# Kernel optimization log

Hardware: AMD Instinct MI355X
Metric: run time of the kernel (lower is better)

The kernel has to match this reference:

```python
import jax, jax.numpy as jnp
import numpy as np

N = 128      # n_ab: number of independent tiny MLPs
H = 128      # hidden width
L = 4097     # odd alpha grid length, alpha[L//2] == pi/2


def setup_inputs() -> dict:
    key = jax.random.key(0)
    ks = jax.random.split(key, 10)
    alpha = jnp.linspace(0.0, np.pi, L).astype(jnp.float32)
    s = 1.0 / np.sqrt(H)
    w0 = jax.random.normal(ks[0], (N, H, 1), dtype=jnp.float32) * 0.5
    w1 = jax.random.normal(ks[1], (N, H, H), dtype=jnp.float32) * s
    w2 = jax.random.normal(ks[2], (N, H, H), dtype=jnp.float32) * s
    w3 = jax.random.normal(ks[3], (N, 1, H), dtype=jnp.float32) * s
    b0 = jax.random.normal(ks[4], (N, H), dtype=jnp.float32) * 0.1
    b1 = jax.random.normal(ks[5], (N, H), dtype=jnp.float32) * 0.1
    b2 = jax.random.normal(ks[6], (N, H), dtype=jnp.float32) * 0.1
    b3 = jax.random.normal(ks[7], (N, 1), dtype=jnp.float32) * 0.1 + 1.0
    sqrt_a = jax.random.uniform(ks[8], (N,), dtype=jnp.float32, minval=0.5, maxval=1.5)
    return dict(alpha=alpha, w0=w0, w1=w1, w2=w2, w3=w3,
                b0=b0, b1=b1, b2=b2, b3=b3, sqrt_a=sqrt_a)


def _mlp_b(alpha_half, ws, bs):
    # alpha_half: (B,) -> b: (N, B)
    n = ws[0].shape[0]
    x = jnp.broadcast_to(alpha_half[None, :, None], (n, alpha_half.shape[0], 1))
    for w, b in zip(ws[:-1], bs[:-1]):
        x = jax.nn.relu(jnp.einsum('Nij,NBj->NBi', w, x) + b[:, None, :])
    x = jnp.einsum('Nij,NBj->NBi', ws[-1], x) + bs[-1][:, None, :]
    return jnp.square(x)[..., 0]  # (N, B)


def reference(alpha, w0, w1, w2, w3, b0, b1, b2, b3, sqrt_a):
    half = alpha[: alpha.shape[0] // 2 + 1]  # first half incl. pi/2
    ws, bs = (w0, w1, w2, w3), (b0, b1, b2, b3)
    # db/dalpha via jvp with unit tangent: each b[n, j] depends only on
    # alpha_half[j], matching the torch double-autograd trick through z.
    b, db = jax.jvp(lambda a: _mlp_b(a, ws, bs), (half,), (jnp.ones_like(half),))
    b_full = jnp.concatenate([b, b[:, :-1][:, ::-1]], axis=1)          # (N, L)
    db_full = jnp.concatenate([db, -db[:, :-1][:, ::-1]], axis=1)      # (N, L)
    a_full = jnp.square(sqrt_a)[:, None]                               # (N, 1)
    al = alpha[None, :]                                                # (1, L)
    xp = a_full * (jnp.cos(al) - 1.0)
    yp = b_full * jnp.sin(al)
    xp_prime = jnp.broadcast_to(-a_full * jnp.sin(al), b_full.shape)
    yp_prime = b_full * jnp.cos(al) + db_full * jnp.sin(al)
    return xp, yp, xp_prime, yp_prime
```

## Files before the change

kernel.cpp:

```cpp
#include <hip/hip_runtime.h>
#include <math.h>

#define NN 128
#define HH 128
#define LL 4097
#define PH 2049
#define BP2 32
#define NT2 65
#define BP 64
#define NTILE 33
#define WS_NEEDED (2u * 128u * 64u * 64u * 16u)

typedef short bf16x8 __attribute__((ext_vector_type(8)));
typedef float f32x4  __attribute__((ext_vector_type(4)));
typedef unsigned int u32;

__device__ __forceinline__ void split1(float x, u32& hi, u32& lo) {
    u32 bx = __float_as_uint(x);
    hi = bx >> 16;
    float hf = __uint_as_float(bx & 0xffff0000u);
    float d  = x - hf;
    lo = (__float_as_uint(d) + 0x8000u) >> 16;
}

__device__ __forceinline__ u32 cvtpk(float a, float b) {
    u32 r;
    asm("v_cvt_pk_bf16_f32 %0, %1, %2" : "=v"(r) : "v"(a), "v"(b));
    return r;
}

__device__ __forceinline__ void split_pair(float x0, float x1, u32& hpk, u32& lpk) {
    hpk = cvtpk(x0, x1);
    const float h0 = __uint_as_float(hpk << 16);
    const float h1 = __uint_as_float(hpk & 0xffff0000u);
    lpk = cvtpk(x0 - h0, x1 - h1);
}

__device__ __forceinline__ f32x4 MF(bf16x8 a, bf16x8 b, f32x4 c) {
    return __builtin_amdgcn_mfma_f32_16x16x32_bf16(a, b, c, 0, 0, 0);
}


__global__ __launch_bounds__(512) void presplit2(
    const float* __restrict__ w1, const float* __restrict__ w2, uint4* __restrict__ ws)
{
    __shared__ float lw[128 * 132];
    const int b = blockIdx.x;
    const int m = b >> 7, n = b & 127;
    const float* wn = (m ? w2 : w1) + n * HH * HH;
    uint4* dst = ws + b * 4096;
    const int tid = threadIdx.x;

#pragma unroll
    for (int j = 0; j < 8; ++j) {
        const int flat = tid + j * 512;
        const float4 v4 = *(const float4*)(wn + flat * 4);
        const int row = flat >> 5;
        const int col = (flat & 31) * 4;
        *(float4*)(lw + row * 132 + col) = v4;
    }
    __syncthreads();

#pragma unroll
    for (int it = 0; it < 4; ++it) {
        const int s  = tid + it * 512;
        const int l  = s & 63;
        const int fq = s >> 6;
        const int ks = fq & 3, it7 = fq >> 2;
        const int i  = it7 * 16 + (l & 15);
        const int k0 = ks * 32 + (l >> 4) * 8;
        const float* src = lw + i * 132 + k0;
        u32 hd[4], ld_[4];
#pragma unroll
        for (int q = 0; q < 4; ++q)
            split_pair(src[2*q], src[2*q+1], hd[q], ld_[q]);
        dst[(fq*2 + 0)*64 + l] = make_uint4(hd[0], hd[1], hd[2], hd[3]);
        dst[(fq*2 + 1)*64 + l] = make_uint4(ld_[0], ld_[1], ld_[2], ld_[3]);
    }
}

__device__ __forceinline__ void loadW16(const bf16x8* __restrict__ Wf, bf16x8 Wreg[16],
                                        int rq, int l) {
#pragma unroll
    for (int itl = 0; itl < 2; ++itl)
#pragma unroll
        for (int ks = 0; ks < 4; ++ks)
#pragma unroll
            for (int hl = 0; hl < 2; ++hl)
                Wreg[(itl*4 + ks)*2 + hl] = Wf[((((rq*2 + itl)*4 + ks)*2 + hl))*64 + l];
}

__device__ __forceinline__ void gemm_q(const bf16x8 Wreg[16], const char* Xb,
                                       f32x4 acc[2][4], int l) {
    const bf16x8* Xf = (const bf16x8*)Xb;
#pragma unroll
    for (int ks = 0; ks < 4; ++ks) {
        bf16x8 Bh[4], Bl[4];
#pragma unroll
        for (int ct = 0; ct < 4; ++ct) {
            Bh[ct] = Xf[((ct*4 + ks)*2 + 0)*64 + l];
            Bl[ct] = Xf[((ct*4 + ks)*2 + 1)*64 + l];
        }
#pragma unroll
        for (int itl = 0; itl < 2; ++itl) {
            const bf16x8 Ah = Wreg[(itl*4 + ks)*2 + 0];
            const bf16x8 Al = Wreg[(itl*4 + ks)*2 + 1];
#pragma unroll
            for (int ct = 0; ct < 4; ++ct) {
                acc[itl][ct] = MF(Ah, Bh[ct], acc[itl][ct]);
                acc[itl][ct] = MF(Ah, Bl[ct], acc[itl][ct]);
                acc[itl][ct] = MF(Al, Bh[ct], acc[itl][ct]);
            }
        }
    }
}

__global__ __launch_bounds__(256, 4) void sofa_mfma6(
    const float* __restrict__ alpha,
    const float* __restrict__ w0, const float* __restrict__ w3,
    const float* __restrict__ b0, const float* __restrict__ b1,
    const float* __restrict__ b2, const float* __restrict__ b3,
    const float* __restrict__ sqrt_a,
    const uint4* __restrict__ ws,
    float* __restrict__ out)
{
    __shared__ char smem[32768];
    char*  Xb  = smem;
    float* red = (float*)smem;

    const int tile = blockIdx.x, n = blockIdx.y;
    const int tid = threadIdx.x;
    const int l   = tid & 63;
    const int rq  = __builtin_amdgcn_readfirstlane(tid >> 6);
    const int t   = l >> 4;

    const bf16x8* W1f = (const bf16x8*)(ws + n * 4096);
    const bf16x8* W2f = (const bf16x8*)(ws + (128 + n) * 4096);

    bf16x8 Wreg[16];
    loadW16(W1f, Wreg, rq, l);

    {
        const float* w0n = w0 + n * HH;
        const float* b0n = b0 + n * HH;
        const int c  = tid & 63;
        const int jb = tid >> 6;
        int p = tile * BP2 + (c & 31);
        if (p > 2048) p = 2048;
        const float a = alpha[p];
        const bool isdh = c >= 32;
        const int ct = c >> 4;
#pragma unroll
        for (int g8 = 0; g8 < 4; ++g8) {
            const float4 wv4a = *(const float4*)(w0n + jb*32 + g8*8);
            const float4 wv4b = *(const float4*)(w0n + jb*32 + g8*8 + 4);
            const float4 bv4a = *(const float4*)(b0n + jb*32 + g8*8);
            const float4 bv4b = *(const float4*)(b0n + jb*32 + g8*8 + 4);
            const float wvv[8] = {wv4a.x,wv4a.y,wv4a.z,wv4a.w,wv4b.x,wv4b.y,wv4b.z,wv4b.w};
            const float bvv[8] = {bv4a.x,bv4a.y,bv4a.z,bv4a.w,bv4b.x,bv4b.y,bv4b.z,bv4b.w};
            u32 hd[4], ld_[4];
#pragma unroll
            for (int q = 0; q < 4; ++q) {
                float vv[2];
#pragma unroll
                for (int e = 0; e < 2; ++e) {
                    const float wv  = wvv[q*2 + e];
                    const float pre = fmaf(wv, a, bvv[q*2 + e]);
                    const bool  on  = pre > 0.f;
                    vv[e] = isdh ? (on ? wv : 0.f) : (on ? pre : 0.f);
                }
                split_pair(vv[0], vv[1], hd[q], ld_[q]);
            }
            const int lane = g8 * 16 + (c & 15);
            const int fq   = ct * 4 + jb;
            *(uint4*)(Xb + ((fq*2 + 0)*64 + lane)*16) = make_uint4(hd[0], hd[1], hd[2], hd[3]);
            *(uint4*)(Xb + ((fq*2 + 1)*64 + lane)*16) = make_uint4(ld_[0], ld_[1], ld_[2], ld_[3]);
        }
    }
    __syncthreads();

    f32x4 acc[2][4];
#pragma unroll
    for (int i0 = 0; i0 < 2; ++i0)
#pragma unroll
        for (int c0 = 0; c0 < 4; ++c0) { f32x4 z = {0.f,0.f,0.f,0.f}; acc[i0][c0] = z; }
    __builtin_amdgcn_s_setprio(1);
    gemm_q(Wreg, Xb, acc, l);
    __builtin_amdgcn_s_setprio(0);

    loadW16(W2f, Wreg, rq, l);

    u32 pxh[2][2][2][2], pxd[2][2][2][2];
    {
        const float* b1n = b1 + n * HH;
#pragma unroll
        for (int itl = 0; itl < 2; ++itl) {
            const int ibase = (rq*2 + itl)*16 + t*4;
#pragma unroll
            for (int c = 0; c < 2; ++c) {
                float hv[4], dv[4];
#pragma unroll
                for (int r = 0; r < 4; ++r) {
                    const float pre = acc[itl][c][r] + b1n[ibase + r];
                    const bool  on  = pre > 0.f;
                    hv[r] = on ? pre : 0.f;
                    dv[r] = on ? acc[itl][c + 2][r] : 0.f;
                }
                split_pair(hv[0], hv[1], pxh[itl][c][0][0], pxh[itl][c][1][0]);
                split_pair(hv[2], hv[3], pxh[itl][c][0][1], pxh[itl][c][1][1]);
                split_pair(dv[0], dv[1], pxd[itl][c][0][0], pxd[itl][c][1][0]);
                split_pair(dv[2], dv[3], pxd[itl][c][0][1], pxd[itl][c][1][1]);
            }
        }
    }
    __syncthreads();

    {
#pragma unroll
        for (int itl = 0; itl < 2; ++itl) {
            const int lane = (itl*2 + (t >> 1))*16 + (l & 15);
            const int off8 = (t & 1)*8;
#pragma unroll
            for (int c = 0; c < 2; ++c) {
#pragma unroll
                for (int hl = 0; hl < 2; ++hl) {
                    uint2 vh; vh.x = pxh[itl][c][hl][0]; vh.y = pxh[itl][c][hl][1];
                    *(uint2*)(Xb + (((c    )*4 + rq)*2 + hl)*1024 + lane*16 + off8) = vh;
                    uint2 vd; vd.x = pxd[itl][c][hl][0]; vd.y = pxd[itl][c][hl][1];
                    *(uint2*)(Xb + (((c + 2)*4 + rq)*2 + hl)*1024 + lane*16 + off8) = vd;
                }
            }
        }
    }
    __syncthreads();

    f32x4 acc2[2][4];
#pragma unroll
    for (int i0 = 0; i0 < 2; ++i0)
#pragma unroll
        for (int c0 = 0; c0 < 4; ++c0) { f32x4 z = {0.f,0.f,0.f,0.f}; acc2[i0][c0] = z; }
    __builtin_amdgcn_s_setprio(1);
    gemm_q(Wreg, Xb, acc2, l);
    __builtin_amdgcn_s_setprio(0);

    float sh[2] = {0.f, 0.f}, sd[2] = {0.f, 0.f};
    {
        const float* b2n = b2 + n * HH;
        const float* w3n = w3 + n * HH;
#pragma unroll
        for (int itl = 0; itl < 2; ++itl) {
            const int ibase = (rq*2 + itl)*16 + t*4;
#pragma unroll
            for (int r = 0; r < 4; ++r) {
                const int   i  = ibase + r;
                const float bv = b2n[i];
                const float wv = w3n[i];
#pragma unroll
                for (int c = 0; c < 2; ++c) {
                    const float pre = acc2[itl][c][r] + bv;
                    const bool  on  = pre > 0.f;
                    sh[c] = fmaf(wv, on ? pre : 0.f,                 sh[c]);
                    sd[c] = fmaf(wv, on ? acc2[itl][c + 2][r] : 0.f, sd[c]);
                }
            }
        }
    }
#pragma unroll
    for (int c = 0; c < 2; ++c) {
        sh[c] += __shfl_xor(sh[c], 16); sh[c] += __shfl_xor(sh[c], 32);
        sd[c] += __shfl_xor(sd[c], 16); sd[c] += __shfl_xor(sd[c], 32);
    }
    __syncthreads();
    if (l < 16) {
#pragma unroll
        for (int c = 0; c < 2; ++c) {
            red[rq * 32 + c * 16 + l]        = sh[c];
            red[128 + rq * 32 + c * 16 + l]  = sd[c];
        }
    }
    __syncthreads();

    if (tid < 32) {
        float oo = b3[n], d2 = 0.f;
#pragma unroll
        for (int q = 0; q < 4; ++q) {
            oo += red[q * 32 + tid];
            d2 += red[128 + q * 32 + tid];
        }
        const float bb = oo * oo;
        const float db = 2.f * oo * d2;
        const float sa = sqrt_a[n];
        const float af = sa * sa;
        const int   NL = NN * LL;
        const int   k1 = tile * BP2 + tid;
        if (k1 < PH) {
            const float al = alpha[k1];
            const float sn = __sinf(al), cs = __cosf(al);
            const int base = n * LL + k1;
            out[base]          = af * (cs - 1.f);
            out[NL + base]     = bb * sn;
            out[2 * NL + base] = -af * sn;
            out[3 * NL + base] = fmaf(bb, cs, db * sn);
            if (k1 <= PH - 2) {
                const int base2 = n * LL + (LL - 1) - k1;
                out[base2]          = af * (-cs - 1.f);
                out[NL + base2]     = bb * sn;
                out[2 * NL + base2] = -af * sn;
                out[3 * NL + base2] = fmaf(bb, -cs, -db * sn);
            }
        }
    }
}


__device__ __forceinline__ void stageW_fb(const float* __restrict__ wn, char* Wb, int tid) {
#pragma unroll
    for (int it = 0; it < 4; ++it) {
        const int s  = tid + it * 512;
        const int l  = s & 63;
        const int fq = s >> 6;
        const int ks = fq & 3, it7 = fq >> 2;
        const int i  = it7 * 16 + (l & 15);
        const int k0 = ks * 32 + (l >> 4) * 8;
        const float4* src = (const float4*)(wn + i * HH + k0);
        const float4 va = src[0], vb = src[1];
        const float v[8] = {va.x, va.y, va.z, va.w, vb.x, vb.y, vb.z, vb.w};
        u32 hd[4], ld_[4];
#pragma unroll
        for (int q = 0; q < 4; ++q) {
            u32 h0, l0, h1, l1;
            split1(v[2*q], h0, l0); split1(v[2*q+1], h1, l1);
            hd[q]  = h0 | (h1 << 16);
            ld_[q] = l0 | (l1 << 16);
        }
        *(uint4*)(Wb + (((fq*2)+0)*64 + l)*16) = make_uint4(hd[0], hd[1], hd[2], hd[3]);
        *(uint4*)(Wb + (((fq*2)+1)*64 + l)*16) = make_uint4(ld_[0], ld_[1], ld_[2], ld_[3]);
    }
}

__device__ __forceinline__ void gemm128_fb(const char* Wb, const char* Xb,
                                           f32x4 acc[4][2], int rw, int cw, int l) {
    const bf16x8* Wf = (const bf16x8*)Wb;
    const bf16x8* Xf = (const bf16x8*)Xb;
#pragma unroll
    for (int ks = 0; ks < 4; ++ks) {
        bf16x8 Bh[2], Bl[2];
#pragma unroll
        for (int cg = 0; cg < 2; ++cg) {
            const int ct = cw + cg * 4;
            Bh[cg] = Xf[((ct*4 + ks)*2 + 0)*64 + l];
            Bl[cg] = Xf[((ct*4 + ks)*2 + 1)*64 + l];
        }
#pragma unroll
        for (int itl = 0; itl < 4; ++itl) {
            const int IT = rw * 4 + itl;
            const bf16x8 Ah = Wf[((IT*4 + ks)*2 + 0)*64 + l];
            const bf16x8 Al = Wf[((IT*4 + ks)*2 + 1)*64 + l];
#pragma unroll
            for (int cg = 0; cg < 2; ++cg) {
                acc[itl][cg] = MF(Ah, Bh[cg], acc[itl][cg]);
                acc[itl][cg] = MF(Ah, Bl[cg], acc[itl][cg]);
                acc[itl][cg] = MF(Al, Bh[cg], acc[itl][cg]);
            }
        }
    }
}

__global__ __launch_bounds__(512, 2) void sofa_mfma_fb(
    const float* __restrict__ alpha,
    const float* __restrict__ w0, const float* __restrict__ w1,
    const float* __restrict__ w2, const float* __restrict__ w3,
    const float* __restrict__ b0, const float* __restrict__ b1,
    const float* __restrict__ b2, const float* __restrict__ b3,
    const float* __restrict__ sqrt_a,
    float* __restrict__ out)
{
    __shared__ char smem[131072];
    char* Wb = smem;
    char* Xb = smem + 65536;
    float* red = (float*)smem;

    const int tile = blockIdx.x, n = blockIdx.y;
    const int tid = threadIdx.x;
    const int l   = tid & 63;
    const int w   = tid >> 6;
    const int rw  = w & 1;
    const int cw  = w >> 1;
    const int t   = l >> 4;

    stageW_fb(w1 + n * HH * HH, Wb, tid);
    {
        const float* w0n = w0 + n * HH;
        const float* b0n = b0 + n * HH;
        const int c  = tid & 127;
        const int jb = tid >> 7;
        int p = tile * BP + (c & 63);
        if (p > 2048) p = 2048;
        const float a = alpha[p];
        const bool isdh = c >= 64;
        const int ct = c >> 4;
#pragma unroll
        for (int g8 = 0; g8 < 4; ++g8) {
            u32 hd[4], ld_[4];
#pragma unroll
            for (int q = 0; q < 4; ++q) {
                float vv[2];
#pragma unroll
                for (int e = 0; e < 2; ++e) {
                    const int j = jb * 32 + g8 * 8 + q * 2 + e;
                    const float wv  = w0n[j];
                    const float pre = fmaf(wv, a, b0n[j]);
                    const bool  on  = pre > 0.f;
                    vv[e] = isdh ? (on ? wv : 0.f) : (on ? pre : 0.f);
                }
                u32 h0, l0, h1, l1;
                split1(vv[0], h0, l0); split1(vv[1], h1, l1);
                hd[q]  = h0 | (h1 << 16);
                ld_[q] = l0 | (l1 << 16);
            }
            const int lane = g8 * 16 + (c & 15);
            const int fq   = ct * 4 + jb;
            *(uint4*)(Xb + ((fq*2 + 0)*64 + lane)*16) = make_uint4(hd[0], hd[1], hd[2], hd[3]);
            *(uint4*)(Xb + ((fq*2 + 1)*64 + lane)*16) = make_uint4(ld_[0], ld_[1], ld_[2], ld_[3]);
        }
    }
    __syncthreads();

    f32x4 acc[4][2];
#pragma unroll
    for (int i0 = 0; i0 < 4; ++i0)
#pragma unroll
        for (int c0 = 0; c0 < 2; ++c0) { f32x4 z = {0.f,0.f,0.f,0.f}; acc[i0][c0] = z; }
    gemm128_fb(Wb, Xb, acc, rw, cw, l);

    u32 px[4][2][2][2];
    {
        const float* b1n = b1 + n * HH;
#pragma unroll
        for (int itl = 0; itl < 4; ++itl) {
            const int ibase = (rw*4 + itl)*16 + t*4;
            float hv[4], dv[4];
#pragma unroll
            for (int r = 0; r < 4; ++r) {
                const float pre = acc[itl][0][r] + b1n[ibase + r];
                const bool  on  = pre > 0.f;
                hv[r] = on ? pre : 0.f;
                dv[r] = on ? acc[itl][1][r] : 0.f;
            }
#pragma unroll
            for (int cg = 0; cg < 2; ++cg) {
                const float* vs = cg ? dv : hv;
                u32 a0,c0,a1,c1,a2,c2,a3,c3;
                split1(vs[0],a0,c0); split1(vs[1],a1,c1);
                split1(vs[2],a2,c2); split1(vs[3],a3,c3);
                px[itl][cg][0][0] = a0 | (a1 << 16);
                px[itl][cg][0][1] = a2 | (a3 << 16);
                px[itl][cg][1][0] = c0 | (c1 << 16);
                px[itl][cg][1][1] = c2 | (c3 << 16);
            }
        }
    }
    __syncthreads();

    stageW_fb(w2 + n * HH * HH, Wb, tid);
    {
#pragma unroll
        for (int itl = 0; itl < 4; ++itl) {
            const int IT   = rw*4 + itl;
            const int lane = ((IT & 1)*2 + (t >> 1))*16 + (l & 15);
            const int off8 = (t & 1)*8;
            const int ksn  = IT >> 1;
#pragma unroll
            for (int cg = 0; cg < 2; ++cg) {
                const int fq = (cw + cg*4)*4 + ksn;
#pragma unroll
                for (int hl = 0; hl < 2; ++hl) {
                    uint2 vv; vv.x = px[itl][cg][hl][0]; vv.y = px[itl][cg][hl][1];
                    *(uint2*)(Xb + ((fq*2 + hl)*64 + lane)*16 + off8) = vv;
                }
            }
        }
    }
    __syncthreads();

    f32x4 acc2[4][2];
#pragma unroll
    for (int i0 = 0; i0 < 4; ++i0)
#pragma unroll
        for (int c0 = 0; c0 < 2; ++c0) { f32x4 z = {0.f,0.f,0.f,0.f}; acc2[i0][c0] = z; }
    gemm128_fb(Wb, Xb, acc2, rw, cw, l);

    float sh = 0.f, sd = 0.f;
    {
        const float* b2n = b2 + n * HH;
        const float* w3n = w3 + n * HH;
#pragma unroll
        for (int itl = 0; itl < 4; ++itl) {
            const int ibase = (rw*4 + itl)*16 + t*4;
#pragma unroll
            for (int r = 0; r < 4; ++r) {
                const int   i   = ibase + r;
                const float pre = acc2[itl][0][r] + b2n[i];
                const bool  on  = pre > 0.f;
                const float hv  = on ? pre : 0.f;
                const float dv  = on ? acc2[itl][1][r] : 0.f;
                const float wv  = w3n[i];
                sh = fmaf(wv, hv, sh);
                sd = fmaf(wv, dv, sd);
            }
        }
    }
    sh += __shfl_xor(sh, 16); sh += __shfl_xor(sh, 32);
    sd += __shfl_xor(sd, 16); sd += __shfl_xor(sd, 32);
    __syncthreads();
    if (t == 0) {
        const int p = cw * 16 + (l & 15);
        red[rw * 64 + p]        = sh;
        red[128 + rw * 64 + p]  = sd;
    }
    __syncthreads();

    if (tid < 64) {
        const float oo = b3[n] + red[tid] + red[64 + tid];
        const float d2 = red[128 + tid] + red[192 + tid];
        const float bb = oo * oo;
        const float db = 2.f * oo * d2;
        const float sa = sqrt_a[n];
        const float af = sa * sa;
        const int   NL = NN * LL;
        const int   k1 = tile * BP + tid;
        if (k1 < PH) {
            {
                const float al = alpha[k1];
                const float sn = sinf(al), cs = cosf(al);
                const int base = n * LL + k1;
                out[base]          = af * (cs - 1.f);
                out[NL + base]     = bb * sn;
                out[2 * NL + base] = -af * sn;
                out[3 * NL + base] = fmaf(bb, cs, db * sn);
            }
            if (k1 <= PH - 2) {
                const int   k2  = (LL - 1) - k1;
                const float al2 = alpha[k2];
                const float sn2 = sinf(al2), cs2 = cosf(al2);
                const int base2 = n * LL + k2;
                out[base2]          = af * (cs2 - 1.f);
                out[NL + base2]     = bb * sn2;
                out[2 * NL + base2] = -af * sn2;
                out[3 * NL + base2] = fmaf(bb, cs2, -db * sn2);
            }
        }
    }
}

extern "C" void kernel_launch(void* const* d_in, const int* in_sizes, int n_in,
                              void* d_out, int out_size, void* d_ws, size_t ws_size,
                              hipStream_t stream) {
    const float* alpha  = (const float*)d_in[0];
    const float* w0     = (const float*)d_in[1];
    const float* w1     = (const float*)d_in[2];
    const float* w2     = (const float*)d_in[3];
    const float* w3     = (const float*)d_in[4];
    const float* b0     = (const float*)d_in[5];
    const float* b1     = (const float*)d_in[6];
    const float* b2     = (const float*)d_in[7];
    const float* b3     = (const float*)d_in[8];
    const float* sqrt_a = (const float*)d_in[9];
    (void)in_sizes; (void)n_in; (void)out_size;

    if (ws_size >= (size_t)WS_NEEDED) {
        uint4* ws = (uint4*)d_ws;
        presplit2<<<256, 512, 0, stream>>>(w1, w2, ws);
        dim3 grid(NT2, NN);
        sofa_mfma6<<<grid, 256, 0, stream>>>(alpha, w0, w3, b0, b1, b2, b3,
                                             sqrt_a, ws, (float*)d_out);
    } else {
        dim3 grid(NTILE, NN);
        sofa_mfma_fb<<<grid, 512, 0, stream>>>(alpha, w0, w1, w2, w3,
                                               b0, b1, b2, b3, sqrt_a,
                                               (float*)d_out);
    }
}
```

Measured before the change: 179.5 us.

## Process two alpha sub-tiles per block with interleaved GEMM stages

Each block now handles 64 alpha points as two 32-point halves in separate LDS buffers. It reuses each loaded weight register set (W1, then W2) for both halves and interleaves the halves' stages, so elementwise packing of one half overlaps the MFMA GEMM of the other. This halves the grid and the per-point cost of reloading the bf16-split weights from the workspace. In exchange, LDS per block doubles to 64KB and launch bounds drop to 2 blocks per CU, which reduces occupancy and latency hiding.

```diff
diff --git a/kernel.cpp b/kernel.cpp
--- a/kernel.cpp
+++ b/kernel.cpp
@@ -5,8 +5,7 @@
 #define HH 128
 #define LL 4097
 #define PH 2049
-#define BP2 32
-#define NT2 65
+#define NT3 33
 #define BP 64
 #define NTILE 33
 #define WS_NEEDED (2u * 128u * 64u * 64u * 16u)
@@ -115,153 +114,110 @@
     }
 }
 
-__global__ __launch_bounds__(256, 4) void sofa_mfma6(
-    const float* __restrict__ alpha,
-    const float* __restrict__ w0, const float* __restrict__ w3,
-    const float* __restrict__ b0, const float* __restrict__ b1,
-    const float* __restrict__ b2, const float* __restrict__ b3,
-    const float* __restrict__ sqrt_a,
-    const uint4* __restrict__ ws,
-    float* __restrict__ out)
-{
-    __shared__ char smem[32768];
-    char*  Xb  = smem;
-    float* red = (float*)smem;
-
-    const int tile = blockIdx.x, n = blockIdx.y;
-    const int tid = threadIdx.x;
-    const int l   = tid & 63;
-    const int rq  = __builtin_amdgcn_readfirstlane(tid >> 6);
-    const int t   = l >> 4;
-
-    const bf16x8* W1f = (const bf16x8*)(ws + n * 4096);
-    const bf16x8* W2f = (const bf16x8*)(ws + (128 + n) * 4096);
-
-    bf16x8 Wreg[16];
-    loadW16(W1f, Wreg, rq, l);
-
-    {
-        const float* w0n = w0 + n * HH;
-        const float* b0n = b0 + n * HH;
-        const int c  = tid & 63;
-        const int jb = tid >> 6;
-        int p = tile * BP2 + (c & 31);
-        if (p > 2048) p = 2048;
-        const float a = alpha[p];
-        const bool isdh = c >= 32;
-        const int ct = c >> 4;
-#pragma unroll
-        for (int g8 = 0; g8 < 4; ++g8) {
-            const float4 wv4a = *(const float4*)(w0n + jb*32 + g8*8);
-            const float4 wv4b = *(const float4*)(w0n + jb*32 + g8*8 + 4);
-            const float4 bv4a = *(const float4*)(b0n + jb*32 + g8*8);
-            const float4 bv4b = *(const float4*)(b0n + jb*32 + g8*8 + 4);
-            const float wvv[8] = {wv4a.x,wv4a.y,wv4a.z,wv4a.w,wv4b.x,wv4b.y,wv4b.z,wv4b.w};
-            const float bvv[8] = {bv4a.x,bv4a.y,bv4a.z,bv4a.w,bv4b.x,bv4b.y,bv4b.z,bv4b.w};
-            u32 hd[4], ld_[4];
-#pragma unroll
-            for (int q = 0; q < 4; ++q) {
-                float vv[2];
-#pragma unroll
-                for (int e = 0; e < 2; ++e) {
-                    const float wv  = wvv[q*2 + e];
-                    const float pre = fmaf(wv, a, bvv[q*2 + e]);
-                    const bool  on  = pre > 0.f;
-                    vv[e] = isdh ? (on ? wv : 0.f) : (on ? pre : 0.f);
-                }
-                split_pair(vv[0], vv[1], hd[q], ld_[q]);
-            }
-            const int lane = g8 * 16 + (c & 15);
-            const int fq   = ct * 4 + jb;
-            *(uint4*)(Xb + ((fq*2 + 0)*64 + lane)*16) = make_uint4(hd[0], hd[1], hd[2], hd[3]);
-            *(uint4*)(Xb + ((fq*2 + 1)*64 + lane)*16) = make_uint4(ld_[0], ld_[1], ld_[2], ld_[3]);
-        }
-    }
-    __syncthreads();
-
-    f32x4 acc[2][4];
-#pragma unroll
-    for (int i0 = 0; i0 < 2; ++i0)
-#pragma unroll
-        for (int c0 = 0; c0 < 4; ++c0) { f32x4 z = {0.f,0.f,0.f,0.f}; acc[i0][c0] = z; }
-    __builtin_amdgcn_s_setprio(1);
-    gemm_q(Wreg, Xb, acc, l);
-    __builtin_amdgcn_s_setprio(0);
-
-    loadW16(W2f, Wreg, rq, l);
-
-    u32 pxh[2][2][2][2], pxd[2][2][2][2];
-    {
-        const float* b1n = b1 + n * HH;
-#pragma unroll
-        for (int itl = 0; itl < 2; ++itl) {
-            const int ibase = (rq*2 + itl)*16 + t*4;
+__device__ __forceinline__ void layer0_half(
+    const float* __restrict__ w0n, const float* __restrict__ b0n,
+    const float* __restrict__ alpha, int pbase, char* Xb, int tid)
+{
+    const int c  = tid & 63;
+    const int jb = tid >> 6;
+    int p = pbase + (c & 31);
+    if (p > 2048) p = 2048;
+    const float a = alpha[p];
+    const bool isdh = c >= 32;
+    const int ct = c >> 4;
+#pragma unroll
+    for (int g8 = 0; g8 < 4; ++g8) {
+        const float4 wv4a = *(const float4*)(w0n + jb*32 + g8*8);
+        const float4 wv4b = *(const float4*)(w0n + jb*32 + g8*8 + 4);
+        const float4 bv4a = *(const float4*)(b0n + jb*32 + g8*8);
+        const float4 bv4b = *(const float4*)(b0n + jb*32 + g8*8 + 4);
+        const float wvv[8] = {wv4a.x,wv4a.y,wv4a.z,wv4a.w,wv4b.x,wv4b.y,wv4b.z,wv4b.w};
+        const float bvv[8] = {bv4a.x,bv4a.y,bv4a.z,bv4a.w,bv4b.x,bv4b.y,bv4b.z,bv4b.w};
+        u32 hd[4], ld_[4];
+#pragma unroll
+        for (int q = 0; q < 4; ++q) {
+            float vv[2];
+#pragma unroll
+            for (int e = 0; e < 2; ++e) {
+                const float wv  = wvv[q*2 + e];
+                const float pre = fmaf(wv, a, bvv[q*2 + e]);
+                const bool  on  = pre > 0.f;
+                vv[e] = isdh ? (on ? wv : 0.f) : (on ? pre : 0.f);
+            }
+            split_pair(vv[0], vv[1], hd[q], ld_[q]);
+        }
+        const int lane = g8 * 16 + (c & 15);
+        const int fq   = ct * 4 + jb;
+        *(uint4*)(Xb + ((fq*2 + 0)*64 + lane)*16) = make_uint4(hd[0], hd[1], hd[2], hd[3]);
+        *(uint4*)(Xb + ((fq*2 + 1)*64 + lane)*16) = make_uint4(ld_[0], ld_[1], ld_[2], ld_[3]);
+    }
+}
+
+__device__ __forceinline__ void T_pack(
+    const f32x4 acc[2][4], const float* __restrict__ b1n, int rq, int t,
+    u32 pxh[2][2][2][2], u32 pxd[2][2][2][2])
+{
+#pragma unroll
+    for (int itl = 0; itl < 2; ++itl) {
+        const int ibase = (rq*2 + itl)*16 + t*4;
+#pragma unroll
+        for (int c = 0; c < 2; ++c) {
+            float hv[4], dv[4];
+#pragma unroll
+            for (int r = 0; r < 4; ++r) {
+                const float pre = acc[itl][c][r] + b1n[ibase + r];
+                const bool  on  = pre > 0.f;
+                hv[r] = on ? pre : 0.f;
+                dv[r] = on ? acc[itl][c + 2][r] : 0.f;
+            }
+            split_pair(hv[0], hv[1], pxh[itl][c][0][0], pxh[itl][c][1][0]);
+            split_pair(hv[2], hv[3], pxh[itl][c][0][1], pxh[itl][c][1][1]);
+            split_pair(dv[0], dv[1], pxd[itl][c][0][0], pxd[itl][c][1][0]);
+            split_pair(dv[2], dv[3], pxd[itl][c][0][1], pxd[itl][c][1][1]);
+        }
+    }
+}
+
+__device__ __forceinline__ void writeX2(
+    const u32 pxh[2][2][2][2], const u32 pxd[2][2][2][2],
+    char* Xb, int rq, int t, int l)
+{
+#pragma unroll
+    for (int itl = 0; itl < 2; ++itl) {
+        const int lane = (itl*2 + (t >> 1))*16 + (l & 15);
+        const int off8 = (t & 1)*8;
+#pragma unroll
+        for (int c = 0; c < 2; ++c) {
+#pragma unroll
+            for (int hl = 0; hl < 2; ++hl) {
+                uint2 vh; vh.x = pxh[itl][c][hl][0]; vh.y = pxh[itl][c][hl][1];
+                *(uint2*)(Xb + (((c    )*4 + rq)*2 + hl)*1024 + lane*16 + off8) = vh;
+                uint2 vd; vd.x = pxd[itl][c][hl][0]; vd.y = pxd[itl][c][hl][1];
+                *(uint2*)(Xb + (((c + 2)*4 + rq)*2 + hl)*1024 + lane*16 + off8) = vd;
+            }
+        }
+    }
+}
+
+__device__ __forceinline__ void L3_red(
+    const f32x4 acc2[2][4], const float* __restrict__ b2n,
+    const float* __restrict__ w3n, int rq, int t, int l, float* red)
+{
+    float sh[2] = {0.f, 0.f}, sd[2] = {0.f, 0.f};
+#pragma unroll
+    for (int itl = 0; itl < 2; ++itl) {
+        const int ibase = (rq*2 + itl)*16 + t*4;
+#pragma unroll
+        for (int r = 0; r < 4; ++r) {
+            const int   i  = ibase + r;
+            const float bv = b2n[i];
+            const float wv = w3n[i];
 #pragma unroll
             for (int c = 0; c < 2; ++c) {
-                float hv[4], dv[4];
-#pragma unroll
-                for (int r = 0; r < 4; ++r) {
-                    const float pre = acc[itl][c][r] + b1n[ibase + r];
-                    const bool  on  = pre > 0.f;
-                    hv[r] = on ? pre : 0.f;
-                    dv[r] = on ? acc[itl][c + 2][r] : 0.f;
-                }
-                split_pair(hv[0], hv[1], pxh[itl][c][0][0], pxh[itl][c][1][0]);
-                split_pair(hv[2], hv[3], pxh[itl][c][0][1], pxh[itl][c][1][1]);
-                split_pair(dv[0], dv[1], pxd[itl][c][0][0], pxd[itl][c][1][0]);
-                split_pair(dv[2], dv[3], pxd[itl][c][0][1], pxd[itl][c][1][1]);
-            }
-        }
-    }
-    __syncthreads();
-
-    {
-#pragma unroll
-        for (int itl = 0; itl < 2; ++itl) {
-            const int lane = (itl*2 + (t >> 1))*16 + (l & 15);
-            const int off8 = (t & 1)*8;
-#pragma unroll
-            for (int c = 0; c < 2; ++c) {
-#pragma unroll
-                for (int hl = 0; hl < 2; ++hl) {
-                    uint2 vh; vh.x = pxh[itl][c][hl][0]; vh.y = pxh[itl][c][hl][1];
-                    *(uint2*)(Xb + (((c    )*4 + rq)*2 + hl)*1024 + lane*16 + off8) = vh;
-                    uint2 vd; vd.x = pxd[itl][c][hl][0]; vd.y = pxd[itl][c][hl][1];
-                    *(uint2*)(Xb + (((c + 2)*4 + rq)*2 + hl)*1024 + lane*16 + off8) = vd;
-                }
-            }
-        }
-    }
-    __syncthreads();
-
-    f32x4 acc2[2][4];
-#pragma unroll
-    for (int i0 = 0; i0 < 2; ++i0)
-#pragma unroll
-        for (int c0 = 0; c0 < 4; ++c0) { f32x4 z = {0.f,0.f,0.f,0.f}; acc2[i0][c0] = z; }
-    __builtin_amdgcn_s_setprio(1);
-    gemm_q(Wreg, Xb, acc2, l);
-    __builtin_amdgcn_s_setprio(0);
-
-    float sh[2] = {0.f, 0.f}, sd[2] = {0.f, 0.f};
-    {
-        const float* b2n = b2 + n * HH;
-        const float* w3n = w3 + n * HH;
-#pragma unroll
-        for (int itl = 0; itl < 2; ++itl) {
-            const int ibase = (rq*2 + itl)*16 + t*4;
-#pragma unroll
-            for (int r = 0; r < 4; ++r) {
-                const int   i  = ibase + r;
-                const float bv = b2n[i];
-                const float wv = w3n[i];
-#pragma unroll
-                for (int c = 0; c < 2; ++c) {
-                    const float pre = acc2[itl][c][r] + bv;
-                    const bool  on  = pre > 0.f;
-                    sh[c] = fmaf(wv, on ? pre : 0.f,                 sh[c]);
-                    sd[c] = fmaf(wv, on ? acc2[itl][c + 2][r] : 0.f, sd[c]);
-                }
+                const float pre = acc2[itl][c][r] + bv;
+                const bool  on  = pre > 0.f;
+                sh[c] = fmaf(wv, on ? pre : 0.f,                 sh[c]);
+                sd[c] = fmaf(wv, on ? acc2[itl][c + 2][r] : 0.f, sd[c]);
             }
         }
     }
@@ -270,7 +226,6 @@
         sh[c] += __shfl_xor(sh[c], 16); sh[c] += __shfl_xor(sh[c], 32);
         sd[c] += __shfl_xor(sd[c], 16); sd[c] += __shfl_xor(sd[c], 32);
     }
-    __syncthreads();
     if (l < 16) {
 #pragma unroll
         for (int c = 0; c < 2; ++c) {
@@ -278,8 +233,13 @@
             red[128 + rq * 32 + c * 16 + l]  = sd[c];
         }
     }
-    __syncthreads();
-
+}
+
+__device__ __forceinline__ void epi(
+    const float* red, int tid, int n, int k1base,
+    const float* __restrict__ alpha, const float* __restrict__ b3,
+    const float* __restrict__ sqrt_a, float* __restrict__ out)
+{
     if (tid < 32) {
         float oo = b3[n], d2 = 0.f;
 #pragma unroll
@@ -292,7 +252,7 @@
         const float sa = sqrt_a[n];
         const float af = sa * sa;
         const int   NL = NN * LL;
-        const int   k1 = tile * BP2 + tid;
+        const int   k1 = k1base + tid;
         if (k1 < PH) {
             const float al = alpha[k1];
             const float sn = __sinf(al), cs = __cosf(al);
@@ -310,6 +270,103 @@
             }
         }
     }
+}
+
+__global__ __launch_bounds__(256, 2) void sofa_mfma7(
+    const float* __restrict__ alpha,
+    const float* __restrict__ w0, const float* __restrict__ w3,
+    const float* __restrict__ b0, const float* __restrict__ b1,
+    const float* __restrict__ b2, const float* __restrict__ b3,
+    const float* __restrict__ sqrt_a,
+    const uint4* __restrict__ ws,
+    float* __restrict__ out)
+{
+    __shared__ char smem[65536];
+    char* XbA = smem;
+    char* XbB = smem + 32768;
+    float* redA = (float*)XbA;
+    float* redB = (float*)XbB;
+
+    const int tile = blockIdx.x, n = blockIdx.y;
+    const int tid = threadIdx.x;
+    const int l   = tid & 63;
+    const int rq  = __builtin_amdgcn_readfirstlane(tid >> 6);
+    const int t   = l >> 4;
+    const int pA  = tile * 64;
+    const int pB  = tile * 64 + 32;
+
+    const float* w0n = w0 + n * HH;
+    const float* b0n = b0 + n * HH;
+    const float* b1n = b1 + n * HH;
+    const float* b2n = b2 + n * HH;
+    const float* w3n = w3 + n * HH;
+    const bf16x8* W1f = (const bf16x8*)(ws + n * 4096);
+    const bf16x8* W2f = (const bf16x8*)(ws + (128 + n) * 4096);
+
+    bf16x8 Wreg[16];
+    loadW16(W1f, Wreg, rq, l);
+
+    layer0_half(w0n, b0n, alpha, pA, XbA, tid);
+    __syncthreads();
+
+    f32x4 accA[2][4];
+#pragma unroll
+    for (int i0 = 0; i0 < 2; ++i0)
+#pragma unroll
+        for (int c0 = 0; c0 < 4; ++c0) { f32x4 z = {0.f,0.f,0.f,0.f}; accA[i0][c0] = z; }
+    __builtin_amdgcn_s_setprio(1);
+    gemm_q(Wreg, XbA, accA, l);
+    __builtin_amdgcn_s_setprio(0);
+    layer0_half(w0n, b0n, alpha, pB, XbB, tid);
+    __syncthreads();
+
+    f32x4 accB[2][4];
+#pragma unroll
+    for (int i0 = 0; i0 < 2; ++i0)
+#pragma unroll
+        for (int c0 = 0; c0 < 4; ++c0) { f32x4 z = {0.f,0.f,0.f,0.f}; accB[i0][c0] = z; }
+    __builtin_amdgcn_s_setprio(1);
+    gemm_q(Wreg, XbB, accB, l);
+    __builtin_amdgcn_s_setprio(0);
+    {
+        u32 pxh[2][2][2][2], pxd[2][2][2][2];
+        T_pack(accA, b1n, rq, t, pxh, pxd);
+        writeX2(pxh, pxd, XbA, rq, t, l);
+    }
+    loadW16(W2f, Wreg, rq, l);
+    __syncthreads();
+
+    f32x4 acc2A[2][4];
+#pragma unroll
+    for (int i0 = 0; i0 < 2; ++i0)
+#pragma unroll
+        for (int c0 = 0; c0 < 4; ++c0) { f32x4 z = {0.f,0.f,0.f,0.f}; acc2A[i0][c0] = z; }
+    __builtin_amdgcn_s_setprio(1);
+    gemm_q(Wreg, XbA, acc2A, l);
+    __builtin_amdgcn_s_setprio(0);
+    {
+        u32 pxh[2][2][2][2], pxd[2][2][2][2];
+        T_pack(accB, b1n, rq, t, pxh, pxd);
+        writeX2(pxh, pxd, XbB, rq, t, l);
+    }
+    __syncthreads();
+
+    f32x4 acc2B[2][4];
+#pragma unroll
+    for (int i0 = 0; i0 < 2; ++i0)
+#pragma unroll
+        for (int c0 = 0; c0 < 4; ++c0) { f32x4 z = {0.f,0.f,0.f,0.f}; acc2B[i0][c0] = z; }
+    __builtin_amdgcn_s_setprio(1);
+    gemm_q(Wreg, XbB, acc2B, l);
+    __builtin_amdgcn_s_setprio(0);
+    L3_red(acc2A, b2n, w3n, rq, t, l, redA);
+    __syncthreads();
+
+    epi(redA, tid, n, pA, alpha, b3, sqrt_a, out);
+    L3_red(acc2B, b2n, w3n, rq, t, l, redB);
+    __syncthreads();
+
+    epi(redB, tid, n, pB, alpha, b3, sqrt_a, out);
 }
 
 
@@ -571,8 +628,8 @@
     if (ws_size >= (size_t)WS_NEEDED) {
         uint4* ws = (uint4*)d_ws;
         presplit2<<<256, 512, 0, stream>>>(w1, w2, ws);
-        dim3 grid(NT2, NN);
-        sofa_mfma6<<<grid, 256, 0, stream>>>(alpha, w0, w3, b0, b1, b2, b3,
+        dim3 grid(NT3, NN);
+        sofa_mfma7<<<grid, 256, 0, stream>>>(alpha, w0, w3, b0, b1, b2, b3,
                                              sqrt_a, ws, (float*)d_out);
     } else {
         dim3 grid(NTILE, NN);
```

Measured after the change: 191.7 us. +6.8%, slower.
